# Kernel tuning notes

Hardware: AMD Instinct MI355X
Metric: run time of the kernel (lower is better)

Reference implementation:

```python
import jax, jax.numpy as jnp
import numpy as np

NUM_HEADS = 16
HIDDEN = 1024
HEAD_DIM = HIDDEN // NUM_HEADS


def setup_inputs() -> dict:
    key = jax.random.key(0)
    ks = jax.random.split(key, 12)
    B, S, H = 4, 1024, HIDDEN
    s = 1.0 / np.sqrt(H)
    inp = {
        "aspect_hidden": jax.random.normal(ks[0], (B, S, H), jnp.float32),
        "opinion_hidden": jax.random.normal(ks[1], (B, S, H), jnp.float32),
        "attention_mask": jnp.ones((B, S), jnp.int32),
        # torch nn.Linear weights are [out, in]
        "Wq": jax.random.normal(ks[2], (H, H), jnp.float32) * s,
        "bq": jnp.zeros((H,), jnp.float32),
        "Wk": jax.random.normal(ks[3], (H, H), jnp.float32) * s,
        "bk": jnp.zeros((H,), jnp.float32),
        "Wv": jax.random.normal(ks[4], (H, H), jnp.float32) * s,
        "bv": jnp.zeros((H,), jnp.float32),
        "Wo": jax.random.normal(ks[5], (H, H), jnp.float32) * s,
        "bo": jnp.zeros((H,), jnp.float32),
        # nn.Bilinear(H, H, 1): weight [1, H, H], bias [1]
        "Wbil": jax.random.normal(ks[6], (1, H, H), jnp.float32) * s,
        "bbil": jnp.zeros((1,), jnp.float32),
    }
    return inp


def reference(aspect_hidden, opinion_hidden, attention_mask,
              Wq, bq, Wk, bk, Wv, bv, Wo, bo, Wbil, bbil):
    B, Sq, H = aspect_hidden.shape
    Sk = opinion_hidden.shape[1]
    nh, hd = NUM_HEADS, HEAD_DIM
    scale = hd ** (-0.5)

    q = (aspect_hidden @ Wq.T + bq).reshape(B, Sq, nh, hd).transpose(0, 2, 1, 3)
    k = (opinion_hidden @ Wk.T + bk).reshape(B, Sk, nh, hd).transpose(0, 2, 1, 3)
    v = (opinion_hidden @ Wv.T + bv).reshape(B, Sk, nh, hd).transpose(0, 2, 1, 3)

    # bilinear span bias: span[b,s] = a[b,s] @ Wbil[0] @ o[b,s] + bbil
    span = jnp.einsum('bsh,hk,bsk->bs', aspect_hidden, Wbil[0], opinion_hidden) + bbil[0]

    # scores [B, nh, Sq, Sk] with span bias broadcast over heads and keys
    scores = jnp.einsum('bhqd,bhkd->bhqk', q, k) * scale + span[:, None, :, None]
    scores = jnp.where(attention_mask[:, None, None, :] == 0, -jnp.inf, scores)

    probs = jax.nn.softmax(scores, axis=-1)
    ctx = jnp.einsum('bhqk,bhkd->bhqd', probs, v)
    ctx = ctx.transpose(0, 2, 1, 3).reshape(B, Sq, H)
    return ctx @ Wo.T + bo
```

## Files before the change

### kernel.cpp

```cpp
#include <hip/hip_runtime.h>
#include <hip/hip_bf16.h>
#include <stdint.h>

typedef __attribute__((ext_vector_type(4))) float f32x4;
typedef __attribute__((ext_vector_type(16))) float f32x16;
typedef __attribute__((ext_vector_type(8))) short bf16x8;
typedef __attribute__((ext_vector_type(4))) unsigned int u32x4;
typedef __attribute__((ext_vector_type(2))) unsigned int u32x2;
typedef unsigned short u16;

#define GBL_AS1(p) ((const __attribute__((address_space(1))) void*)(p))
#define LDS_AS3(p) ((__attribute__((address_space(3))) void*)(p))

static __device__ __forceinline__ u16 f2bf(float f) {
  __hip_bfloat16 h = __float2bfloat16(f);
  union { __hip_bfloat16 h; u16 u; } c; c.h = h;
  return c.u;
}

__global__ __launch_bounds__(256) void cast_weights(
    const float* __restrict__ wq_, const float* __restrict__ wk_,
    const float* __restrict__ wv_, const float* __restrict__ wo_,
    const int* __restrict__ mask,
    u16* __restrict__ WqB, u16* __restrict__ WkB,
    u16* __restrict__ WvB, u16* __restrict__ WoB,
    int* __restrict__ flags) {
  if (blockIdx.x == 0 && threadIdx.x < 64) {
    int bb = threadIdx.x >> 4, kt = threadIdx.x & 15;
    int anyz = 0;
    for (int s = 0; s < 64; ++s) anyz |= (mask[bb * 1024 + kt * 64 + s] == 0);
    flags[threadIdx.x] = anyz;
  }
  int idx = blockIdx.x * 256 + threadIdx.x;
#pragma unroll
  for (int j = 0; j < 4; ++j) {
    int i = idx + j * 262144;
    int w = i >> 18, off = i & 262143;
    const float* src = (w == 0) ? wq_ : (w == 1) ? wk_ : (w == 2) ? wv_ : wo_;
    u16* dst = (w == 0) ? WqB : (w == 1) ? WkB : (w == 2) ? WvB : WoB;
    float4 v = reinterpret_cast<const float4*>(src)[off];
    ushort4 ov;
    ov.x = f2bf(v.x); ov.y = f2bf(v.y); ov.z = f2bf(v.z); ov.w = f2bf(v.w);
    reinterpret_cast<ushort4*>(dst)[off] = ov;
  }
}

static __device__ __forceinline__ void gemm_core(const u16* __restrict__ Atile,
                                                 const u16* __restrict__ Btile,
                                                 u16* lds_a, u16* lds_b,
                                                 f32x4 acc[4][4]) {
  const int tid = threadIdx.x;
  const int lane = tid & 63;
  const int wv = tid >> 6;
  const int wm = wv >> 1, wn = wv & 1;
  const int fr = lane & 15, fq = lane >> 4;
  for (int kt = 0; kt < 32; ++kt) {
#pragma unroll
    for (int i = 0; i < 2; ++i) {
      const int cb = (wv * 2 + i) * 64;
      const int c = cb + lane;
      const int row = c >> 2;
      const int off = (c & 3) * 8;
      __builtin_amdgcn_global_load_lds(GBL_AS1(Atile + (size_t)row * 1024 + kt * 32 + off),
                                       LDS_AS3(lds_a + cb * 8), 16, 0, 0);
      __builtin_amdgcn_global_load_lds(GBL_AS1(Btile + (size_t)row * 1024 + kt * 32 + off),
                                       LDS_AS3(lds_b + cb * 8), 16, 0, 0);
    }
    __syncthreads();
    bf16x8 af[4], bfv[4];
#pragma unroll
    for (int mi = 0; mi < 4; ++mi)
      af[mi] = *(const bf16x8*)&lds_a[(wm * 64 + mi * 16 + fr) * 32 + fq * 8];
#pragma unroll
    for (int ni = 0; ni < 4; ++ni)
      bfv[ni] = *(const bf16x8*)&lds_b[(wn * 64 + ni * 16 + fr) * 32 + fq * 8];
#pragma unroll
    for (int mi = 0; mi < 4; ++mi)
#pragma unroll
      for (int ni = 0; ni < 4; ++ni)
        acc[mi][ni] = __builtin_amdgcn_mfma_f32_16x16x32_bf16(af[mi], bfv[ni], acc[mi][ni], 0, 0, 0);
    __syncthreads();
  }
}

static __device__ __forceinline__ void gemm_core_f32a(const float* __restrict__ A32,
                                                      const u16* __restrict__ Btile,
                                                      u16* lds_a, u16* lds_b,
                                                      f32x4 acc[4][4]) {
  const int tid = threadIdx.x;
  const int lane = tid & 63;
  const int wv = tid >> 6;
  const int wm = wv >> 1, wn = wv & 1;
  const int fr = lane & 15, fq = lane >> 4;
  for (int kt = 0; kt < 32; ++kt) {
    float4 a0[2], a1[2];
#pragma unroll
    for (int i = 0; i < 2; ++i) {
      const int c = (wv * 2 + i) * 64 + lane;
      const int row = c >> 2;
      const int off = (c & 3) * 8;
      const float* s = A32 + (size_t)row * 1024 + kt * 32 + off;
      a0[i] = *(const float4*)s;
      a1[i] = *(const float4*)(s + 4);
    }
#pragma unroll
    for (int i = 0; i < 2; ++i) {
      const int cb = (wv * 2 + i) * 64;
      const int c = cb + lane;
      const int row = c >> 2;
      const int off = (c & 3) * 8;
      __builtin_amdgcn_global_load_lds(GBL_AS1(Btile + (size_t)row * 1024 + kt * 32 + off),
                                       LDS_AS3(lds_b + cb * 8), 16, 0, 0);
    }
#pragma unroll
    for (int i = 0; i < 2; ++i) {
      const int c = (wv * 2 + i) * 64 + lane;
      unsigned int w0, w1, w2, w3;
      asm("v_cvt_pk_bf16_f32 %0, %1, %2" : "=v"(w0) : "v"(a0[i].x), "v"(a0[i].y));
      asm("v_cvt_pk_bf16_f32 %0, %1, %2" : "=v"(w1) : "v"(a0[i].z), "v"(a0[i].w));
      asm("v_cvt_pk_bf16_f32 %0, %1, %2" : "=v"(w2) : "v"(a1[i].x), "v"(a1[i].y));
      asm("v_cvt_pk_bf16_f32 %0, %1, %2" : "=v"(w3) : "v"(a1[i].z), "v"(a1[i].w));
      *(u32x4*)&lds_a[c * 8] = (u32x4){w0, w1, w2, w3};
    }
    __syncthreads();
    bf16x8 af[4], bfv[4];
#pragma unroll
    for (int mi = 0; mi < 4; ++mi)
      af[mi] = *(const bf16x8*)&lds_a[(wm * 64 + mi * 16 + fr) * 32 + fq * 8];
#pragma unroll
    for (int ni = 0; ni < 4; ++ni)
      bfv[ni] = *(const bf16x8*)&lds_b[(wn * 64 + ni * 16 + fr) * 32 + fq * 8];
#pragma unroll
    for (int mi = 0; mi < 4; ++mi)
#pragma unroll
      for (int ni = 0; ni < 4; ++ni)
        acc[mi][ni] = __builtin_amdgcn_mfma_f32_16x16x32_bf16(af[mi], bfv[ni], acc[mi][ni], 0, 0, 0);
    __syncthreads();
  }
}

__global__ __launch_bounds__(256) void qkv_gemm(
    const float* __restrict__ aspect32, const float* __restrict__ opinion32,
    const u16* __restrict__ Wq, const u16* __restrict__ Wk, const u16* __restrict__ Wv,
    const float* __restrict__ bq, const float* __restrict__ bk, const float* __restrict__ bv,
    u16* __restrict__ q_ws, u16* __restrict__ k_ws, u16* __restrict__ vt_ws) {
  __shared__ __align__(16) u16 lds_a[128 * 32];
  __shared__ __align__(16) u16 lds_b[128 * 32];
  const int mt = blockIdx.x;
  const int nt = blockIdx.y;
  const int w = nt >> 3, ntl = nt & 7;
  const float* A32 = (w == 0) ? aspect32 : opinion32;
  const u16* W = (w == 0) ? Wq : (w == 1) ? Wk : Wv;
  const float* bias = (w == 0) ? bq : (w == 1) ? bk : bv;
  f32x4 acc[4][4];
#pragma unroll
  for (int i = 0; i < 4; ++i)
#pragma unroll
    for (int j = 0; j < 4; ++j) acc[i][j] = (f32x4){0.f, 0.f, 0.f, 0.f};
  gemm_core_f32a(A32 + (size_t)mt * 128 * 1024, W + (size_t)ntl * 128 * 1024,
                 lds_a, lds_b, acc);
  const int lane = threadIdx.x & 63, wvi = threadIdx.x >> 6;
  const int wm = wvi >> 1, wn = wvi & 1, fr = lane & 15, fq = lane >> 4;
  u16* dst01 = (w == 0) ? q_ws : k_ws;
  const float qscl = (w == 0) ? 0.18033688f : 1.0f;
#pragma unroll
  for (int mi = 0; mi < 4; ++mi)
#pragma unroll
    for (int ni = 0; ni < 4; ++ni)
#pragma unroll
      for (int r = 0; r < 4; ++r) {
        int m = mt * 128 + wm * 64 + mi * 16 + fq * 4 + r;
        int nl = ntl * 128 + wn * 64 + ni * 16 + fr;
        float v = (acc[mi][ni][r] + bias[nl]) * qscl;
        int b = m >> 10, s = m & 1023, h = nl >> 6, d = nl & 63;
        u16 u = f2bf(v);
        if (w < 2) dst01[(((size_t)(b * 16 + h)) * 1024 + s) * 64 + d] = u;
        else       vt_ws[(((size_t)(b * 16 + h)) * 64 + d) * 1024 + s] = u;
      }
}

__global__ __launch_bounds__(256, 4) void attn_kernel(
    const u16* __restrict__ q_ws, const u16* __restrict__ k_ws,
    const u16* __restrict__ vt_ws, const int* __restrict__ mask,
    const int* __restrict__ flags, u16* __restrict__ ctx_ws) {
  __shared__ __align__(16) u16 k_lds[2][64 * 64];
  __shared__ __align__(16) u16 vt_lds[2][64 * 64];
  __shared__ __align__(16) float scl_lds[4][32];
  const int bid = blockIdx.x;
  const int bh = bid & 63, qt = bid >> 6;
  const int b = bh >> 4, h = bh & 15;
  const int tid = threadIdx.x, lane = tid & 63, wv = tid >> 6;
  const int l31 = lane & 31, hi = lane >> 5;
  const u16* qbase = q_ws + (size_t)bh * 65536 + (size_t)qt * 8192;
  const u16* kbase = k_ws + (size_t)bh * 65536;
  const u16* vtbase = vt_ws + (size_t)bh * 65536;

#define STAGE_KV(kt_, buf_) do { \
    _Pragma("unroll") \
    for (int i_ = 0; i_ < 2; ++i_) { \
      int cb_ = (wv * 2 + i_) * 64; \
      int c_ = cb_ + lane; \
      int r_ = c_ >> 3; \
      int sc_ = ((c_ & 7) ^ (r_ & 7)) * 8; \
      __builtin_amdgcn_global_load_lds(GBL_AS1(kbase + (size_t)((kt_) * 64 + r_) * 64 + sc_), \
                                       LDS_AS3(&k_lds[buf_][cb_ * 8]), 16, 0, 0); \
      __builtin_amdgcn_global_load_lds(GBL_AS1(vtbase + (size_t)r_ * 1024 + (kt_) * 64 + sc_), \
                                       LDS_AS3(&vt_lds[buf_][cb_ * 8]), 16, 0, 0); \
    } \
  } while (0)

  {
    u16* qstage = &k_lds[0][0];
#pragma unroll
    for (int i_ = 0; i_ < 4; ++i_) {
      int cb_ = (wv * 4 + i_) * 64;
      int c_ = cb_ + lane;
      int r_ = c_ >> 3;
      int sc_ = ((c_ & 7) ^ (r_ & 7)) * 8;
      __builtin_amdgcn_global_load_lds(GBL_AS1(qbase + (size_t)r_ * 64 + sc_),
                                       LDS_AS3(qstage + cb_ * 8), 16, 0, 0);
    }
  }
  __syncthreads();
  bf16x8 qf[4];
  {
    int rq = wv * 32 + l31;
    const u16* qr = &k_lds[0][0] + rq * 64;
    int rx = rq & 7;
#pragma unroll
    for (int ds = 0; ds < 4; ++ds)
      qf[ds] = *(const bf16x8*)&qr[((ds * 2 + hi) ^ rx) * 8];
  }
  __syncthreads();
  STAGE_KV(0, 0);
  __syncthreads();

  f32x16 ctx0, ctx1;
#pragma unroll
  for (int z = 0; z < 16; ++z) { ctx0[z] = 0.f; ctx1[z] = 0.f; }
  float psum_half = 0.f;

  for (int kt = 0; kt < 16; ++kt) {
    const int cur = kt & 1;
    if (kt < 15) STAGE_KV(kt + 1, cur ^ 1);

    f32x16 sc[2];
#pragma unroll
    for (int kb = 0; kb < 2; ++kb) {
      f32x16 a;
#pragma unroll
      for (int z = 0; z < 16; ++z) a[z] = 0.f;
      int r = kb * 32 + l31;
      const u16* kr = &k_lds[cur][r * 64];
      int rx = r & 7;
#pragma unroll
      for (int ds = 0; ds < 4; ++ds) {
        bf16x8 kf = *(const bf16x8*)&kr[((ds * 2 + hi) ^ rx) * 8];
        a = __builtin_amdgcn_mfma_f32_32x32x16_bf16(kf, qf[ds], a, 0, 0, 0);
      }
      sc[kb] = a;
    }

    if (flags[b * 16 + kt]) {
#pragma unroll
      for (int kb = 0; kb < 2; ++kb)
#pragma unroll
        for (int r2 = 0; r2 < 16; ++r2) {
          int key = kb * 32 + (r2 & 3) + 8 * (r2 >> 2) + 4 * hi;
          if (mask[b * 1024 + kt * 64 + key] == 0) sc[kb][r2] = -30000.0f;
        }
    }

#pragma unroll
    for (int kb = 0; kb < 2; ++kb)
#pragma unroll
      for (int r2 = 0; r2 < 16; ++r2) {
        float p = __builtin_exp2f(sc[kb][r2]);
        sc[kb][r2] = p;
        psum_half += p;
      }

#pragma unroll
    for (int kb = 0; kb < 2; ++kb) {
      unsigned int w[8];
#pragma unroll
      for (int j = 0; j < 8; ++j) {
        unsigned int t;
        asm("v_cvt_pk_bf16_f32 %0, %1, %2" : "=v"(t) : "v"(sc[kb][2 * j]), "v"(sc[kb][2 * j + 1]));
        w[j] = t;
      }
      u32x2 a0 = __builtin_amdgcn_permlane32_swap(w[0], w[2], false, false);
      u32x2 a1 = __builtin_amdgcn_permlane32_swap(w[1], w[3], false, false);
      u32x2 a2 = __builtin_amdgcn_permlane32_swap(w[4], w[6], false, false);
      u32x2 a3 = __builtin_amdgcn_permlane32_swap(w[5], w[7], false, false);
      union { u32x4 u; bf16x8 b; } P0, P1;
      P0.u = (u32x4){ a0[0], a1[0], a0[1], a1[1] };
      P1.u = (u32x4){ a2[0], a3[0], a2[1], a3[1] };
#pragma unroll
      for (int db = 0; db < 2; ++db) {
        int rv = db * 32 + l31;
        const u16* vr = &vt_lds[cur][rv * 64];
        int rvx = rv & 7;
        bf16x8 v0 = *(const bf16x8*)&vr[((kb * 4 + hi) ^ rvx) * 8];
        bf16x8 v1 = *(const bf16x8*)&vr[((kb * 4 + 2 + hi) ^ rvx) * 8];
        if (db == 0) {
          ctx0 = __builtin_amdgcn_mfma_f32_32x32x16_bf16(P0.b, v0, ctx0, 0, 0, 0);
          ctx0 = __builtin_amdgcn_mfma_f32_32x32x16_bf16(P1.b, v1, ctx0, 0, 0, 0);
        } else {
          ctx1 = __builtin_amdgcn_mfma_f32_32x32x16_bf16(P0.b, v0, ctx1, 0, 0, 0);
          ctx1 = __builtin_amdgcn_mfma_f32_32x32x16_bf16(P1.b, v1, ctx1, 0, 0, 0);
        }
      }
    }
    __syncthreads();
  }

  float lrow = psum_half + __shfl_xor(psum_half, 32);
  float inv = (lrow > 0.f) ? 1.0f / lrow : 0.f;
  if (hi == 0) scl_lds[wv][l31] = inv;
  asm volatile("s_waitcnt lgkmcnt(0)" ::: "memory");
  const int sbase = qt * 128 + wv * 32;
#pragma unroll
  for (int g = 0; g < 4; ++g) {
    float4 s4 = *(const float4*)&scl_lds[wv][g * 8 + hi * 4];
    const float* sp = (const float*)&s4;
#pragma unroll
    for (int i2 = 0; i2 < 4; ++i2) {
      int s = sbase + g * 8 + hi * 4 + i2;
      size_t rowoff = ((size_t)(b * 1024 + s)) * 1024 + h * 64;
      ctx_ws[rowoff + l31]      = f2bf(ctx0[g * 4 + i2] * sp[i2]);
      ctx_ws[rowoff + 32 + l31] = f2bf(ctx1[g * 4 + i2] * sp[i2]);
    }
  }
#undef STAGE_KV
}

__global__ __launch_bounds__(256) void out_gemm(const u16* __restrict__ ctxB,
                                                const u16* __restrict__ Wo,
                                                const float* __restrict__ bo,
                                                float* __restrict__ out) {
  __shared__ __align__(16) u16 lds_a[128 * 32];
  __shared__ __align__(16) u16 lds_b[128 * 32];
  const int mt = blockIdx.x, nt = blockIdx.y;
  f32x4 acc[4][4];
#pragma unroll
  for (int i = 0; i < 4; ++i)
#pragma unroll
    for (int j = 0; j < 4; ++j) acc[i][j] = (f32x4){0.f, 0.f, 0.f, 0.f};
  gemm_core(ctxB + (size_t)mt * 128 * 1024, Wo + (size_t)nt * 128 * 1024, lds_a, lds_b, acc);
  const int lane = threadIdx.x & 63, wvi = threadIdx.x >> 6;
  const int wm = wvi >> 1, wn = wvi & 1, fr = lane & 15, fq = lane >> 4;
#pragma unroll
  for (int mi = 0; mi < 4; ++mi)
#pragma unroll
    for (int ni = 0; ni < 4; ++ni)
#pragma unroll
      for (int r = 0; r < 4; ++r) {
        int m = mt * 128 + wm * 64 + mi * 16 + fq * 4 + r;
        int n = nt * 128 + wn * 64 + ni * 16 + fr;
        out[(size_t)m * 1024 + n] = acc[mi][ni][r] + bo[n];
      }
}

extern "C" void kernel_launch(void* const* d_in, const int* in_sizes, int n_in,
                              void* d_out, int out_size, void* d_ws, size_t ws_size,
                              hipStream_t stream) {
  const float* aspect = (const float*)d_in[0];
  const float* opinion = (const float*)d_in[1];
  const int* mask = (const int*)d_in[2];
  const float* Wq = (const float*)d_in[3];
  const float* bq = (const float*)d_in[4];
  const float* Wk = (const float*)d_in[5];
  const float* bk = (const float*)d_in[6];
  const float* Wv = (const float*)d_in[7];
  const float* bv = (const float*)d_in[8];
  const float* Wo = (const float*)d_in[9];
  const float* bo = (const float*)d_in[10];
  float* out = (float*)d_out;
  char* ws = (char*)d_ws;

  const size_t MB = 1u << 20;
  u16* WqB   = (u16*)(ws + 16 * MB);
  u16* WkB   = (u16*)(ws + 18 * MB);
  u16* WvB   = (u16*)(ws + 20 * MB);
  u16* WoB   = (u16*)(ws + 22 * MB);
  u16* q_ws  = (u16*)(ws + 24 * MB);
  u16* k_ws  = (u16*)(ws + 32 * MB);
  u16* vt_ws = (u16*)(ws + 40 * MB);
  u16* ctx_ws= (u16*)(ws + 48 * MB);
  int* flags = (int*)(out + out_size - 64);

  cast_weights<<<1024, 256, 0, stream>>>(Wq, Wk, Wv, Wo, mask,
                                         WqB, WkB, WvB, WoB, flags);
  qkv_gemm<<<dim3(32, 24), 256, 0, stream>>>(aspect, opinion, WqB, WkB, WvB,
                                             bq, bk, bv, q_ws, k_ws, vt_ws);
  attn_kernel<<<512, 256, 0, stream>>>(q_ws, k_ws, vt_ws, mask, flags, ctx_ws);
  out_gemm<<<dim3(32, 8), 256, 0, stream>>>(ctx_ws, WoB, bo, out);
}
```

Before: 108.7 us.

## Fuse Q, K and V projections into one block per output tile

The QKV GEMM now computes all three projections in each block, loading each fp32 activation tile once and converting it to bf16 once. The opinion tile is shared between the K and V products. This removes the redundant activation loads and casts that came from using separate blocks per weight matrix. In exchange the grid shrinks from 768 to 256 blocks, and each block holds three accumulator sets and five LDS tiles. Occupancy is pinned to one block per CU via launch bounds, which may underfill the 256 CUs and leave less latency hiding.

```diff
diff --git a/kernel.cpp b/kernel.cpp
--- a/kernel.cpp
+++ b/kernel.cpp
@@ -83,25 +83,50 @@
   }
 }
 
-static __device__ __forceinline__ void gemm_core_f32a(const float* __restrict__ A32,
-                                                      const u16* __restrict__ Btile,
-                                                      u16* lds_a, u16* lds_b,
-                                                      f32x4 acc[4][4]) {
-  const int tid = threadIdx.x;
-  const int lane = tid & 63;
-  const int wv = tid >> 6;
+__global__ __launch_bounds__(256, 1) void qkv_gemm(
+    const float* __restrict__ aspect32, const float* __restrict__ opinion32,
+    const u16* __restrict__ Wq, const u16* __restrict__ Wk, const u16* __restrict__ Wv,
+    const float* __restrict__ bq, const float* __restrict__ bk, const float* __restrict__ bv,
+    u16* __restrict__ q_ws, u16* __restrict__ k_ws, u16* __restrict__ vt_ws) {
+  __shared__ __align__(16) u16 asp_lds[128 * 32];
+  __shared__ __align__(16) u16 opi_lds[128 * 32];
+  __shared__ __align__(16) u16 bq_lds[128 * 32];
+  __shared__ __align__(16) u16 bk_lds[128 * 32];
+  __shared__ __align__(16) u16 bv_lds[128 * 32];
+  const int mt = blockIdx.x, ntl = blockIdx.y;
+  const float* Aa = aspect32 + (size_t)mt * 128 * 1024;
+  const float* Ao = opinion32 + (size_t)mt * 128 * 1024;
+  const u16* Bq = Wq + (size_t)ntl * 128 * 1024;
+  const u16* Bk = Wk + (size_t)ntl * 128 * 1024;
+  const u16* Bv = Wv + (size_t)ntl * 128 * 1024;
+
+  const int tid = threadIdx.x, lane = tid & 63, wv = tid >> 6;
   const int wm = wv >> 1, wn = wv & 1;
   const int fr = lane & 15, fq = lane >> 4;
+
+  f32x4 acc0[4][4], acc1[4][4], acc2[4][4];
+#pragma unroll
+  for (int i = 0; i < 4; ++i)
+#pragma unroll
+    for (int j = 0; j < 4; ++j) {
+      acc0[i][j] = (f32x4){0.f, 0.f, 0.f, 0.f};
+      acc1[i][j] = (f32x4){0.f, 0.f, 0.f, 0.f};
+      acc2[i][j] = (f32x4){0.f, 0.f, 0.f, 0.f};
+    }
+
   for (int kt = 0; kt < 32; ++kt) {
-    float4 a0[2], a1[2];
+    float4 a0[2], a1[2], o0[2], o1[2];
 #pragma unroll
     for (int i = 0; i < 2; ++i) {
       const int c = (wv * 2 + i) * 64 + lane;
       const int row = c >> 2;
       const int off = (c & 3) * 8;
-      const float* s = A32 + (size_t)row * 1024 + kt * 32 + off;
-      a0[i] = *(const float4*)s;
-      a1[i] = *(const float4*)(s + 4);
+      const float* sa = Aa + (size_t)row * 1024 + kt * 32 + off;
+      a0[i] = *(const float4*)sa;
+      a1[i] = *(const float4*)(sa + 4);
+      const float* so = Ao + (size_t)row * 1024 + kt * 32 + off;
+      o0[i] = *(const float4*)so;
+      o1[i] = *(const float4*)(so + 4);
     }
 #pragma unroll
     for (int i = 0; i < 2; ++i) {
@@ -109,8 +134,12 @@
       const int c = cb + lane;
       const int row = c >> 2;
       const int off = (c & 3) * 8;
-      __builtin_amdgcn_global_load_lds(GBL_AS1(Btile + (size_t)row * 1024 + kt * 32 + off),
-                                       LDS_AS3(lds_b + cb * 8), 16, 0, 0);
+      __builtin_amdgcn_global_load_lds(GBL_AS1(Bq + (size_t)row * 1024 + kt * 32 + off),
+                                       LDS_AS3(bq_lds + cb * 8), 16, 0, 0);
+      __builtin_amdgcn_global_load_lds(GBL_AS1(Bk + (size_t)row * 1024 + kt * 32 + off),
+                                       LDS_AS3(bk_lds + cb * 8), 16, 0, 0);
+      __builtin_amdgcn_global_load_lds(GBL_AS1(Bv + (size_t)row * 1024 + kt * 32 + off),
+                                       LDS_AS3(bv_lds + cb * 8), 16, 0, 0);
     }
 #pragma unroll
     for (int i = 0; i < 2; ++i) {
@@ -120,49 +149,49 @@
       asm("v_cvt_pk_bf16_f32 %0, %1, %2" : "=v"(w1) : "v"(a0[i].z), "v"(a0[i].w));
       asm("v_cvt_pk_bf16_f32 %0, %1, %2" : "=v"(w2) : "v"(a1[i].x), "v"(a1[i].y));
       asm("v_cvt_pk_bf16_f32 %0, %1, %2" : "=v"(w3) : "v"(a1[i].z), "v"(a1[i].w));
-      *(u32x4*)&lds_a[c * 8] = (u32x4){w0, w1, w2, w3};
+      *(u32x4*)&asp_lds[c * 8] = (u32x4){w0, w1, w2, w3};
+      asm("v_cvt_pk_bf16_f32 %0, %1, %2" : "=v"(w0) : "v"(o0[i].x), "v"(o0[i].y));
+      asm("v_cvt_pk_bf16_f32 %0, %1, %2" : "=v"(w1) : "v"(o0[i].z), "v"(o0[i].w));
+      asm("v_cvt_pk_bf16_f32 %0, %1, %2" : "=v"(w2) : "v"(o1[i].x), "v"(o1[i].y));
+      asm("v_cvt_pk_bf16_f32 %0, %1, %2" : "=v"(w3) : "v"(o1[i].z), "v"(o1[i].w));
+      *(u32x4*)&opi_lds[c * 8] = (u32x4){w0, w1, w2, w3};
     }
     __syncthreads();
-    bf16x8 af[4], bfv[4];
+
+    bf16x8 afa[4], afo[4], bfv[4];
+#pragma unroll
+    for (int mi = 0; mi < 4; ++mi) {
+      const int r = (wm * 64 + mi * 16 + fr) * 32 + fq * 8;
+      afa[mi] = *(const bf16x8*)&asp_lds[r];
+      afo[mi] = *(const bf16x8*)&opi_lds[r];
+    }
+#pragma unroll
+    for (int ni = 0; ni < 4; ++ni)
+      bfv[ni] = *(const bf16x8*)&bq_lds[(wn * 64 + ni * 16 + fr) * 32 + fq * 8];
 #pragma unroll
     for (int mi = 0; mi < 4; ++mi)
-      af[mi] = *(const bf16x8*)&lds_a[(wm * 64 + mi * 16 + fr) * 32 + fq * 8];
-#pragma unroll
-    for (int ni = 0; ni < 4; ++ni)
-      bfv[ni] = *(const bf16x8*)&lds_b[(wn * 64 + ni * 16 + fr) * 32 + fq * 8];
+#pragma unroll
+      for (int ni = 0; ni < 4; ++ni)
+        acc0[mi][ni] = __builtin_amdgcn_mfma_f32_16x16x32_bf16(afa[mi], bfv[ni], acc0[mi][ni], 0, 0, 0);
+#pragma unroll
+    for (int ni = 0; ni < 4; ++ni)
+      bfv[ni] = *(const bf16x8*)&bk_lds[(wn * 64 + ni * 16 + fr) * 32 + fq * 8];
 #pragma unroll
     for (int mi = 0; mi < 4; ++mi)
 #pragma unroll
       for (int ni = 0; ni < 4; ++ni)
-        acc[mi][ni] = __builtin_amdgcn_mfma_f32_16x16x32_bf16(af[mi], bfv[ni], acc[mi][ni], 0, 0, 0);
+        acc1[mi][ni] = __builtin_amdgcn_mfma_f32_16x16x32_bf16(afo[mi], bfv[ni], acc1[mi][ni], 0, 0, 0);
+#pragma unroll
+    for (int ni = 0; ni < 4; ++ni)
+      bfv[ni] = *(const bf16x8*)&bv_lds[(wn * 64 + ni * 16 + fr) * 32 + fq * 8];
+#pragma unroll
+    for (int mi = 0; mi < 4; ++mi)
+#pragma unroll
+      for (int ni = 0; ni < 4; ++ni)
+        acc2[mi][ni] = __builtin_amdgcn_mfma_f32_16x16x32_bf16(afo[mi], bfv[ni], acc2[mi][ni], 0, 0, 0);
     __syncthreads();
   }
-}
-
-__global__ __launch_bounds__(256) void qkv_gemm(
-    const float* __restrict__ aspect32, const float* __restrict__ opinion32,
-    const u16* __restrict__ Wq, const u16* __restrict__ Wk, const u16* __restrict__ Wv,
-    const float* __restrict__ bq, const float* __restrict__ bk, const float* __restrict__ bv,
-    u16* __restrict__ q_ws, u16* __restrict__ k_ws, u16* __restrict__ vt_ws) {
-  __shared__ __align__(16) u16 lds_a[128 * 32];
-  __shared__ __align__(16) u16 lds_b[128 * 32];
-  const int mt = blockIdx.x;
-  const int nt = blockIdx.y;
-  const int w = nt >> 3, ntl = nt & 7;
-  const float* A32 = (w == 0) ? aspect32 : opinion32;
-  const u16* W = (w == 0) ? Wq : (w == 1) ? Wk : Wv;
-  const float* bias = (w == 0) ? bq : (w == 1) ? bk : bv;
-  f32x4 acc[4][4];
-#pragma unroll
-  for (int i = 0; i < 4; ++i)
-#pragma unroll
-    for (int j = 0; j < 4; ++j) acc[i][j] = (f32x4){0.f, 0.f, 0.f, 0.f};
-  gemm_core_f32a(A32 + (size_t)mt * 128 * 1024, W + (size_t)ntl * 128 * 1024,
-                 lds_a, lds_b, acc);
-  const int lane = threadIdx.x & 63, wvi = threadIdx.x >> 6;
-  const int wm = wvi >> 1, wn = wvi & 1, fr = lane & 15, fq = lane >> 4;
-  u16* dst01 = (w == 0) ? q_ws : k_ws;
-  const float qscl = (w == 0) ? 0.18033688f : 1.0f;
+
 #pragma unroll
   for (int mi = 0; mi < 4; ++mi)
 #pragma unroll
@@ -171,11 +200,11 @@
       for (int r = 0; r < 4; ++r) {
         int m = mt * 128 + wm * 64 + mi * 16 + fq * 4 + r;
         int nl = ntl * 128 + wn * 64 + ni * 16 + fr;
-        float v = (acc[mi][ni][r] + bias[nl]) * qscl;
         int b = m >> 10, s = m & 1023, h = nl >> 6, d = nl & 63;
-        u16 u = f2bf(v);
-        if (w < 2) dst01[(((size_t)(b * 16 + h)) * 1024 + s) * 64 + d] = u;
-        else       vt_ws[(((size_t)(b * 16 + h)) * 64 + d) * 1024 + s] = u;
+        size_t qkoff = (((size_t)(b * 16 + h)) * 1024 + s) * 64 + d;
+        q_ws[qkoff] = f2bf((acc0[mi][ni][r] + bq[nl]) * 0.18033688f);
+        k_ws[qkoff] = f2bf(acc1[mi][ni][r] + bk[nl]);
+        vt_ws[(((size_t)(b * 16 + h)) * 64 + d) * 1024 + s] = f2bf(acc2[mi][ni][r] + bv[nl]);
       }
 }
 
@@ -392,8 +421,8 @@
 
   cast_weights<<<1024, 256, 0, stream>>>(Wq, Wk, Wv, Wo, mask,
                                          WqB, WkB, WvB, WoB, flags);
-  qkv_gemm<<<dim3(32, 24), 256, 0, stream>>>(aspect, opinion, WqB, WkB, WvB,
-                                             bq, bk, bv, q_ws, k_ws, vt_ws);
+  qkv_gemm<<<dim3(32, 8), 256, 0, stream>>>(aspect, opinion, WqB, WkB, WvB,
+                                            bq, bk, bv, q_ws, k_ws, vt_ws);
   attn_kernel<<<512, 256, 0, stream>>>(q_ws, k_ws, vt_ws, mask, flags, ctx_ws);
   out_gemm<<<dim3(32, 8), 256, 0, stream>>>(ctx_ws, WoB, bo, out);
 }
```

Result: slower. 127.3 us (+17.1%).
